# Optimization experiments

Measured on AMD Instinct MI355X. Metric: run time of the kernel, lower is better.

## Reference

```python
import jax, jax.numpy as jnp
import numpy as np

B, T, C = 4, 4096, 1024
NH, DH = 16, 128          # n_head, d_head = d_qkv // n_head
DQKV, DR = 2048, 256      # d_qkv, d_rank


def _uniform(key, shape, bound):
    return jax.random.uniform(key, shape, jnp.float32, -bound, bound)


def setup_inputs() -> dict:
    key = jax.random.key(0)
    k0, k1, k2, k3, k4 = jax.random.split(key, 5)
    # CastedLinear init: bound = sqrt(3) * 0.5 * in_features**-0.5 (same for w1, w2)
    b_qkv = (3 ** 0.5) * 0.5 * C ** (-0.5)
    b_proj = (3 ** 0.5) * 0.5 * DQKV ** (-0.5)
    return {
        "x": jax.random.normal(k0, (B, T, C), jnp.float32),
        "qkv_w1": _uniform(k1, (DR, C), b_qkv),
        "qkv_w2": _uniform(k2, (3 * DQKV, DR), b_qkv),
        "cproj_w1": _uniform(k3, (DR, DQKV), b_proj),
        "cproj_w2": _uniform(k4, (2 * C, DR), b_proj),
    }


def _rmsnorm(x):
    eps = jnp.finfo(x.dtype).eps  # F.rms_norm default eps
    return x * jax.lax.rsqrt(jnp.mean(x * x, axis=-1, keepdims=True) + eps)


def reference(x, qkv_w1, qkv_w2, cproj_w1, cproj_w2):
    Bx, Tx, Cx = x.shape
    # qkv projection with low-rank factorization + relu^2 activation between factors
    h = _rmsnorm(x) @ qkv_w1.T                      # [B,T,DR]
    h = jnp.square(jax.nn.relu(h))
    qkv = (h @ qkv_w2.T).reshape(Bx, Tx, 3 * NH, DH)
    q, k, v = jnp.split(qkv, 3, axis=2)             # each [B,T,NH,DH]
    q, k = _rmsnorm(q), _rmsnorm(k)

    # rotary embedding: half the head dim rotated, second quarter frequencies zero
    quarter = DH // 4
    freq = (1.0 / 1024.0) ** jnp.linspace(0.0, 1.0, quarter)
    freq = jnp.concatenate([freq, jnp.zeros(quarter, freq.dtype)])  # [DH//2]
    theta = jnp.arange(Tx, dtype=jnp.float32)[:, None] * freq[None, :]
    cos = jnp.cos(theta)[None, :, None, :]          # [1,T,1,DH//2]
    sin = jnp.sin(theta)[None, :, None, :]

    def rope(z):
        z1, z2 = jnp.split(z, 2, axis=-1)
        return jnp.concatenate([z1 * cos + z2 * sin, -z1 * sin + z2 * cos], axis=-1)

    q, k = rope(q), rope(k)

    # causal linear attention: sigmoid-gated cumulative sum over time
    y = jax.nn.relu(q) * jnp.cumsum(jax.nn.sigmoid(k) * v, axis=1)  # [B,T,NH,DH]
    y = y.reshape(Bx, Tx, NH * DH)

    # low-rank output projection (no activation), gated residual
    uv = (y @ cproj_w1.T) @ cproj_w2.T              # [B,T,2C]
    u, g = jnp.split(uv, 2, axis=-1)
    return x + u * jax.nn.silu(g)
```

## Files before the change

kernel.cpp:

```cpp
#include <hip/hip_runtime.h>
#include <hip/hip_bf16.h>

#define TB 4
#define TT 4096
#define TC 1024
#define TNH 16
#define TDH 128
#define TDQKV 2048
#define TDR 256
#define RB 4096
#define ROWS (TB*TT)
#define SLAB (RB*128)
#define NSEG 128
#define SEGT 32

typedef __attribute__((ext_vector_type(8))) short bfx8;
typedef __attribute__((ext_vector_type(4))) float fx4;
typedef __attribute__((address_space(1))) const unsigned char GAS;
typedef __attribute__((address_space(3))) unsigned char LAS;

__device__ __forceinline__ unsigned short f2b(float f) {
    unsigned int u = __float_as_uint(f);
    unsigned int r = (u + 0x7fffu + ((u >> 16) & 1u)) >> 16;
    return (unsigned short)r;
}
__device__ __forceinline__ float b2f(unsigned short h) {
    return __uint_as_float(((unsigned int)h) << 16);
}
__device__ __forceinline__ float sigm(float x) {
    return 1.0f / (1.0f + __expf(-x));
}
__device__ __forceinline__ int xcd_swz(int hw, int nwg) {
    int q = nwg >> 3;
    return (hw & 7) * q + (hw >> 3);
}

__global__ __launch_bounds__(256) void setup_all(const float* __restrict__ wq1, unsigned short* __restrict__ w1b,
                                                 const float* __restrict__ wq2, unsigned short* __restrict__ w2b,
                                                 const float* __restrict__ wc1, unsigned short* __restrict__ wp1b,
                                                 const float* __restrict__ wc2, unsigned short* __restrict__ wp2b,
                                                 float* __restrict__ ct, float* __restrict__ st) {
    int blk = blockIdx.x;
    if (blk < 2816) {
        const float* in; unsigned short* out; int base;
        if (blk < 256)       { in = wq1; out = w1b;  base = blk; }
        else if (blk < 1792) { in = wq2; out = w2b;  base = blk - 256; }
        else if (blk < 2304) { in = wc1; out = wp1b; base = blk - 1792; }
        else                 { in = wc2; out = wp2b; base = blk - 2304; }
        int i = (base * 256 + threadIdx.x) * 4;
        float4 v = *(const float4*)(in + i);
        out[i + 0] = f2b(v.x);
        out[i + 1] = f2b(v.y);
        out[i + 2] = f2b(v.z);
        out[i + 3] = f2b(v.w);
    } else {
        int i = (blk - 2816) * 256 + threadIdx.x;
        int t = i >> 5, j = i & 31;
        float fr = exp2f(-10.0f * (float)j / 31.0f);
        float th = (float)t * fr;
        ct[i] = cosf(th);
        st[i] = sinf(th);
    }
}

__global__ __launch_bounds__(256) void rmsnorm_x(const float* __restrict__ x,
                                                 unsigned short* __restrict__ xn) {
    int row = blockIdx.x;
    int tid = threadIdx.x;
    float4 v = *(const float4*)(x + (size_t)row * TC + tid * 4);
    float ss = v.x * v.x + v.y * v.y + v.z * v.z + v.w * v.w;
    #pragma unroll
    for (int o = 32; o > 0; o >>= 1) ss += __shfl_xor(ss, o);
    __shared__ float red[4];
    if ((tid & 63) == 0) red[tid >> 6] = ss;
    __syncthreads();
    float tot = red[0] + red[1] + red[2] + red[3];
    float sc = rsqrtf(tot * (1.0f / TC) + 1.1920929e-7f);
    unsigned short* o = xn + (size_t)row * TC + tid * 4;
    o[0] = f2b(v.x * sc); o[1] = f2b(v.y * sc); o[2] = f2b(v.z * sc); o[3] = f2b(v.w * sc);
}

template <int EPI>
__global__ __launch_bounds__(256) void gemm_bt(const unsigned short* __restrict__ A, int lda,
                                               const unsigned short* __restrict__ Bm,
                                               unsigned short* __restrict__ C, int ldc,
                                               int N, int K) {
    __shared__ unsigned short As[2][128 * 32];
    __shared__ unsigned short Bs[2][128 * 32];
    const int m0 = blockIdx.y * 128;
    const int n0 = blockIdx.x * 128;
    const int tid = threadIdx.x;
    const int lane = tid & 63;
    const int w = tid >> 6;
    const int wr = w >> 1, wc = w & 1;
    const int r16 = lane & 15;
    const int kk = (lane >> 4) * 8;
    const int l4 = lane >> 2;
    const int c8 = (lane & 3) * 8;
    const int nk = K >> 5;
    fx4 acc[4][4] = {};

    auto stage = [&](int buf, int k0) {
        #pragma unroll
        for (int i = 0; i < 2; ++i) {
            int rr = (w + 4 * i) * 16 + l4;
            const unsigned short* ga = A + (size_t)(m0 + rr) * lda + k0 + c8;
            const unsigned short* gb = Bm + (size_t)(n0 + rr) * K + k0 + c8;
            __builtin_amdgcn_global_load_lds((GAS*)ga, (LAS*)&As[buf][(w + 4 * i) * 512], 16, 0, 0);
            __builtin_amdgcn_global_load_lds((GAS*)gb, (LAS*)&Bs[buf][(w + 4 * i) * 512], 16, 0, 0);
        }
    };

    stage(0, 0);
    __syncthreads();
    int buf = 0;
    for (int ks = 0; ks < nk; ++ks) {
        if (ks + 1 < nk) stage(buf ^ 1, (ks + 1) * 32);
        bfx8 af[4], bfr[4];
        #pragma unroll
        for (int mi = 0; mi < 4; mi++) af[mi] = *(const bfx8*)&As[buf][(wr * 64 + mi * 16 + r16) * 32 + kk];
        #pragma unroll
        for (int ni = 0; ni < 4; ni++) bfr[ni] = *(const bfx8*)&Bs[buf][(wc * 64 + ni * 16 + r16) * 32 + kk];
        #pragma unroll
        for (int mi = 0; mi < 4; mi++)
            #pragma unroll
            for (int ni = 0; ni < 4; ni++)
                acc[mi][ni] = __builtin_amdgcn_mfma_f32_16x16x32_bf16(af[mi], bfr[ni], acc[mi][ni], 0, 0, 0);
        __syncthreads();
        buf ^= 1;
    }

    const int rg = lane >> 4;
    #pragma unroll
    for (int mi = 0; mi < 4; mi++)
        #pragma unroll
        for (int ni = 0; ni < 4; ni++) {
            int col = n0 + wc * 64 + ni * 16 + r16;
            #pragma unroll
            for (int r = 0; r < 4; r++) {
                int row = m0 + wr * 64 + mi * 16 + rg * 4 + r;
                float v = acc[mi][ni][r];
                if (EPI == 1) { v = fmaxf(v, 0.0f); v *= v; }
                if (EPI == 2) {
                    int head = col >> 7;
                    C[(size_t)head * SLAB + (size_t)row * 128 + (col & 127)] = f2b(v);
                } else {
                    C[(size_t)row * ldc + col] = f2b(v);
                }
            }
        }
}

template <int EPI, int NX>
__global__ __launch_bounds__(256) void gemm_sk(const unsigned short* __restrict__ A, int lda,
                                               const unsigned short* __restrict__ Bm,
                                               unsigned short* __restrict__ C, int ldc,
                                               int K) {
    __shared__ unsigned short As[2][128 * 32];
    __shared__ unsigned short Bs[2][64 * 32];
    const int lg = xcd_swz(blockIdx.x, gridDim.x);
    const int n0 = (lg % NX) * 64;
    const int m0 = (lg / NX) * 128;
    const int tid = threadIdx.x;
    const int lane = tid & 63;
    const int w = tid >> 6;
    const int wr = w >> 1, wc = w & 1;
    const int r16 = lane & 15;
    const int kk = (lane >> 4) * 8;
    const int l4 = lane >> 2;
    const int c8 = (lane & 3) * 8;
    const int nk = K >> 5;
    fx4 acc[4][2] = {};

    auto stage = [&](int buf, int k0) {
        #pragma unroll
        for (int i = 0; i < 2; ++i) {
            int rr = (w + 4 * i) * 16 + l4;
            const unsigned short* ga = A + (size_t)(m0 + rr) * lda + k0 + c8;
            __builtin_amdgcn_global_load_lds((GAS*)ga, (LAS*)&As[buf][(w + 4 * i) * 512], 16, 0, 0);
        }
        const unsigned short* gb = Bm + (size_t)(n0 + w * 16 + l4) * K + k0 + c8;
        __builtin_amdgcn_global_load_lds((GAS*)gb, (LAS*)&Bs[buf][w * 512], 16, 0, 0);
    };

    stage(0, 0);
    __syncthreads();
    int buf = 0;
    for (int ks = 0; ks < nk; ++ks) {
        if (ks + 1 < nk) stage(buf ^ 1, (ks + 1) * 32);
        bfx8 af[4], bfr[2];
        #pragma unroll
        for (int mi = 0; mi < 4; mi++) af[mi] = *(const bfx8*)&As[buf][(wr * 64 + mi * 16 + r16) * 32 + kk];
        #pragma unroll
        for (int ni = 0; ni < 2; ni++) bfr[ni] = *(const bfx8*)&Bs[buf][(wc * 32 + ni * 16 + r16) * 32 + kk];
        #pragma unroll
        for (int mi = 0; mi < 4; mi++)
            #pragma unroll
            for (int ni = 0; ni < 2; ni++)
                acc[mi][ni] = __builtin_amdgcn_mfma_f32_16x16x32_bf16(af[mi], bfr[ni], acc[mi][ni], 0, 0, 0);
        __syncthreads();
        buf ^= 1;
    }

    const int rg = lane >> 4;
    #pragma unroll
    for (int mi = 0; mi < 4; mi++)
        #pragma unroll
        for (int ni = 0; ni < 2; ni++) {
            int col = n0 + wc * 32 + ni * 16 + r16;
            #pragma unroll
            for (int r = 0; r < 4; r++) {
                int row = m0 + wr * 64 + mi * 16 + rg * 4 + r;
                float v = acc[mi][ni][r];
                if (EPI == 1) { v = fmaxf(v, 0.0f); v *= v; }
                C[(size_t)row * ldc + col] = f2b(v);
            }
        }
}

__global__ __launch_bounds__(256) void gemm4f64(const unsigned short* __restrict__ A,
                                                const unsigned short* __restrict__ Wm,
                                                const float* __restrict__ x,
                                                float* __restrict__ out) {
    __shared__ unsigned short As[2][64 * 32];
    __shared__ unsigned short Bu[2][64 * 32];
    __shared__ unsigned short Bg[2][64 * 32];
    const int hw = blockIdx.y * gridDim.x + blockIdx.x;
    const int lg = xcd_swz(hw, gridDim.x * gridDim.y);
    const int n0 = (lg & 15) * 64;
    const int m0 = (lg >> 4) * 64;
    const int tid = threadIdx.x;
    const int lane = tid & 63;
    const int w = tid >> 6;
    const int wr = w >> 1, wc = w & 1;
    const int r16 = lane & 15;
    const int rg = lane >> 4;
    const int kk = rg * 8;
    const int l4 = lane >> 2;
    const int c8 = (lane & 3) * 8;
    fx4 accu[2][2] = {};
    fx4 accg[2][2] = {};

    auto stage = [&](int buf, int k0) {
        int rr = w * 16 + l4;
        const unsigned short* ga = A + (size_t)(m0 + rr) * TDR + k0 + c8;
        const unsigned short* gu = Wm + (size_t)(n0 + rr) * TDR + k0 + c8;
        const unsigned short* gg = Wm + (size_t)(1024 + n0 + rr) * TDR + k0 + c8;
        __builtin_amdgcn_global_load_lds((GAS*)ga, (LAS*)&As[buf][w * 512], 16, 0, 0);
        __builtin_amdgcn_global_load_lds((GAS*)gu, (LAS*)&Bu[buf][w * 512], 16, 0, 0);
        __builtin_amdgcn_global_load_lds((GAS*)gg, (LAS*)&Bg[buf][w * 512], 16, 0, 0);
    };

    stage(0, 0);
    float xr[2][2][4];
    #pragma unroll
    for (int mi = 0; mi < 2; mi++)
        #pragma unroll
        for (int ni = 0; ni < 2; ni++)
            #pragma unroll
            for (int r = 0; r < 4; r++)
                xr[mi][ni][r] = x[(size_t)(m0 + wr * 32 + mi * 16 + rg * 4 + r) * TC
                                  + n0 + wc * 32 + ni * 16 + r16];
    __syncthreads();
    int buf = 0;
    for (int ks = 0; ks < 8; ++ks) {
        if (ks + 1 < 8) stage(buf ^ 1, (ks + 1) * 32);
        bfx8 af[2], bu[2], bg[2];
        #pragma unroll
        for (int mi = 0; mi < 2; mi++) af[mi] = *(const bfx8*)&As[buf][(wr * 32 + mi * 16 + r16) * 32 + kk];
        #pragma unroll
        for (int ni = 0; ni < 2; ni++) {
            bu[ni] = *(const bfx8*)&Bu[buf][(wc * 32 + ni * 16 + r16) * 32 + kk];
            bg[ni] = *(const bfx8*)&Bg[buf][(wc * 32 + ni * 16 + r16) * 32 + kk];
        }
        #pragma unroll
        for (int mi = 0; mi < 2; mi++)
            #pragma unroll
            for (int ni = 0; ni < 2; ni++) {
                accu[mi][ni] = __builtin_amdgcn_mfma_f32_16x16x32_bf16(af[mi], bu[ni], accu[mi][ni], 0, 0, 0);
                accg[mi][ni] = __builtin_amdgcn_mfma_f32_16x16x32_bf16(af[mi], bg[ni], accg[mi][ni], 0, 0, 0);
            }
        __syncthreads();
        buf ^= 1;
    }

    #pragma unroll
    for (int mi = 0; mi < 2; mi++)
        #pragma unroll
        for (int ni = 0; ni < 2; ni++) {
            int col = n0 + wc * 32 + ni * 16 + r16;
            #pragma unroll
            for (int r = 0; r < 4; r++) {
                int row = m0 + wr * 32 + mi * 16 + rg * 4 + r;
                float u = accu[mi][ni][r];
                float g = accg[mi][ni][r];
                out[(size_t)row * TC + col] = xr[mi][ni][r] + u * (g * sigm(g));
            }
        }
}

__global__ __launch_bounds__(256) void post64(unsigned short* __restrict__ qkv,
                                              const float* __restrict__ ct,
                                              const float* __restrict__ st,
                                              float* __restrict__ part) {
    const int blk = blockIdx.x;
    const int tile = blk & 63, h = blk >> 6;
    const int g = threadIdx.x >> 4, l16 = threadIdx.x & 15;
    const int d0 = l16 * 4;
    unsigned short* qs = qkv + (size_t)h * SLAB;
    unsigned short* ks = qkv + (size_t)(16 + h) * SLAB;
    unsigned short* vs = qkv + (size_t)(32 + h) * SLAB;
    __shared__ float psum[2][16][128];
    float acc0[2][4] = {};
    float acc1[2][4] = {};

    #pragma unroll
    for (int p = 0; p < 4; ++p) {
        const int t = tile * 64 + p * 16 + g;
        const size_t lo = (size_t)t * 128 + d0, hi = lo + 64;
        ushort4 q1 = *(const ushort4*)(qs + lo);
        ushort4 q2 = *(const ushort4*)(qs + hi);
        ushort4 k1 = *(const ushort4*)(ks + lo);
        ushort4 k2 = *(const ushort4*)(ks + hi);
        float qa[8] = {b2f(q1.x), b2f(q1.y), b2f(q1.z), b2f(q1.w),
                       b2f(q2.x), b2f(q2.y), b2f(q2.z), b2f(q2.w)};
        float ka[8] = {b2f(k1.x), b2f(k1.y), b2f(k1.z), b2f(k1.w),
                       b2f(k2.x), b2f(k2.y), b2f(k2.z), b2f(k2.w)};
        float ssq = 0.0f, ssk = 0.0f;
        #pragma unroll
        for (int j = 0; j < 8; ++j) { ssq += qa[j] * qa[j]; ssk += ka[j] * ka[j]; }
        #pragma unroll
        for (int o = 8; o > 0; o >>= 1) {
            ssq += __shfl_xor(ssq, o);
            ssk += __shfl_xor(ssk, o);
        }
        float qsc = rsqrtf(ssq * (1.0f / TDH) + 1.1920929e-7f);
        float ksc = rsqrtf(ssk * (1.0f / TDH) + 1.1920929e-7f);
        float c[4], s[4];
        if (l16 < 8) {
            float4 cv = *(const float4*)(ct + t * 32 + d0);
            float4 sv = *(const float4*)(st + t * 32 + d0);
            c[0] = cv.x; c[1] = cv.y; c[2] = cv.z; c[3] = cv.w;
            s[0] = sv.x; s[1] = sv.y; s[2] = sv.z; s[3] = sv.w;
        } else {
            c[0] = c[1] = c[2] = c[3] = 1.0f;
            s[0] = s[1] = s[2] = s[3] = 0.0f;
        }
        ushort4 v1 = *(const ushort4*)(vs + lo);
        ushort4 v2 = *(const ushort4*)(vs + hi);
        float va[8] = {b2f(v1.x), b2f(v1.y), b2f(v1.z), b2f(v1.w),
                       b2f(v2.x), b2f(v2.y), b2f(v2.z), b2f(v2.w)};
        ushort4 qo1, qo2, po1, po2;
        unsigned short* qo1p = (unsigned short*)&qo1;
        unsigned short* qo2p = (unsigned short*)&qo2;
        unsigned short* po1p = (unsigned short*)&po1;
        unsigned short* po2p = (unsigned short*)&po2;
        const int h2 = p >> 1;
        #pragma unroll
        for (int j = 0; j < 4; ++j) {
            float z1q = qa[j] * qsc, z2q = qa[4 + j] * qsc;
            float z1k = ka[j] * ksc, z2k = ka[4 + j] * ksc;
            float qlo = z1q * c[j] + z2q * s[j];
            float qhi = z2q * c[j] - z1q * s[j];
            float klo = z1k * c[j] + z2k * s[j];
            float khi = z2k * c[j] - z1k * s[j];
            float plo = sigm(klo) * va[j];
            float phi = sigm(khi) * va[4 + j];
            qo1p[j] = f2b(qlo); qo2p[j] = f2b(qhi);
            po1p[j] = f2b(plo); po2p[j] = f2b(phi);
            acc0[h2][j] += plo;
            acc1[h2][j] += phi;
        }
        *(ushort4*)(qs + lo) = qo1;
        *(ushort4*)(qs + hi) = qo2;
        *(ushort4*)(ks + lo) = po1;
        *(ushort4*)(ks + hi) = po2;
    }
    #pragma unroll
    for (int h2 = 0; h2 < 2; ++h2) {
        *(float4*)&psum[h2][g][d0]      = *(float4*)acc0[h2];
        *(float4*)&psum[h2][g][64 + d0] = *(float4*)acc1[h2];
    }
    __syncthreads();
    const int h2 = threadIdx.x >> 7, d = threadIdx.x & 127;
    float tot = 0.0f;
    #pragma unroll
    for (int gg = 0; gg < 16; ++gg) tot += psum[h2][gg][d];
    part[((size_t)h * NSEG + tile * 2 + h2) * 128 + d] = tot;
}

__global__ __launch_bounds__(256) void scanB128(float* __restrict__ part) {
    int idx = blockIdx.x * 256 + threadIdx.x;
    int h = idx >> 7, d = idx & 127;
    float run = 0.0f;
    #pragma unroll 8
    for (int s = 0; s < NSEG; ++s) {
        float* p = part + ((size_t)(h * NSEG + s)) * 128 + d;
        float tv = *p;
        *p = run;
        run += tv;
    }
}

__global__ __launch_bounds__(256) void scanC3(const unsigned short* __restrict__ qkv,
                                              const float* __restrict__ part,
                                              unsigned short* __restrict__ y) {
    const int bseg = blockIdx.x & 7, h = blockIdx.x >> 3;
    const int g = threadIdx.x >> 4, l16 = threadIdx.x & 15;
    const int seg = bseg * 16 + g;
    const int d0 = l16 * 8;
    const unsigned short* qp = qkv + (size_t)h * SLAB;
    const unsigned short* pp = qkv + (size_t)(16 + h) * SLAB;
    float sum[8];
    const float* pb = part + ((size_t)(h * NSEG + seg)) * 128 + d0;
    *(float4*)&sum[0] = *(const float4*)pb;
    *(float4*)&sum[4] = *(const float4*)(pb + 4);
    #pragma unroll 4
    for (int i = 0; i < SEGT; ++i) {
        int t = seg * SEGT + i;
        size_t off = (size_t)t * 128 + d0;
        bfx8 pv = *(const bfx8*)(pp + off);
        bfx8 qv = *(const bfx8*)(qp + off);
        bfx8 ov;
        #pragma unroll
        for (int j = 0; j < 8; ++j) {
            sum[j] += b2f((unsigned short)pv[j]);
            float q = b2f((unsigned short)qv[j]);
            ov[j] = (short)f2b(fmaxf(q, 0.0f) * sum[j]);
        }
        *(bfx8*)(y + (size_t)t * 2048 + h * 128 + d0) = ov;
    }
}

extern "C" void kernel_launch(void* const* d_in, const int* in_sizes, int n_in,
                              void* d_out, int out_size, void* d_ws, size_t ws_size,
                              hipStream_t stream) {
    (void)in_sizes; (void)n_in; (void)out_size; (void)ws_size;
    const float* x    = (const float*)d_in[0];
    const float* wq1  = (const float*)d_in[1];
    const float* wq2  = (const float*)d_in[2];
    const float* wc1  = (const float*)d_in[3];
    const float* wc2  = (const float*)d_in[4];
    float* out = (float*)d_out;

    char* ws = (char*)d_ws;
    size_t off = 0;
    auto alloc = [&](size_t bytes) -> void* {
        off = (off + 255) & ~(size_t)255;
        void* p = ws + off;
        off += bytes;
        return p;
    };
    char* pool = (char*)alloc((size_t)RB * 6144 * 2);
    unsigned short* qkvb = (unsigned short*)pool;
    unsigned short* xn   = (unsigned short*)pool;
    unsigned short* t1   = (unsigned short*)pool;
    unsigned short* hbuf = (unsigned short*)alloc((size_t)ROWS * TDR * 2);
    unsigned short* w1b  = (unsigned short*)alloc((size_t)TDR * TC * 2);
    unsigned short* w2b  = (unsigned short*)alloc((size_t)3 * TDQKV * TDR * 2);
    unsigned short* wp1b = (unsigned short*)alloc((size_t)TDR * TDQKV * 2);
    unsigned short* wp2b = (unsigned short*)alloc((size_t)2 * TC * TDR * 2);
    float* ct   = (float*)alloc((size_t)TT * 32 * 4);
    float* st   = (float*)alloc((size_t)TT * 32 * 4);
    float* part = (float*)alloc((size_t)TNH * NSEG * 128 * 4);
    unsigned short* ybuf = (unsigned short*)d_out;

    setup_all<<<3328, 256, 0, stream>>>(wq1, w1b, wq2, w2b, wc1, wp1b, wc2, wp2b, ct, st);

    rmsnorm_x<<<ROWS, 256, 0, stream>>>(x, xn);
    gemm_sk<1, 4><<<(ROWS / 128) * (TDR / 64), 256, 0, stream>>>(
        xn, TC, w1b, hbuf, TDR, TC);

    for (int b = 0; b < TB; ++b) {
        gemm_bt<2><<<dim3(6144 / 128, RB / 128), 256, 0, stream>>>(
            hbuf + (size_t)b * RB * TDR, TDR, w2b, qkvb, 0, 6144, TDR);
        post64<<<TNH * 64, 256, 0, stream>>>(qkvb, ct, st, part);
        scanB128<<<(TNH * 128) / 256, 256, 0, stream>>>(part);
        scanC3<<<TNH * 8, 256, 0, stream>>>(qkvb, part, ybuf + (size_t)b * RB * 2048);
    }

    gemm_sk<0, 4><<<(ROWS / 128) * (TDR / 64), 256, 0, stream>>>(
        ybuf, 2048, wp1b, t1, TDR, TDQKV);
    gemm4f64<<<dim3(TC / 64, ROWS / 64), 256, 0, stream>>>(t1, wp2b, x, out);
}
```

Measured before the change: 376.9 us.

## Process multiple batches per chunk in qkv/scan pipeline based on workspace size

Parameterizes the per-batch qkv GEMM, post, and scan kernels by a chunk size, so up to four batches are processed per launch when the workspace allows. This cuts the number of launches and gives larger grids, aiming to fill the GPU better and reduce tail effects. The scan resets its running sum every 128 segments to keep batches independent. The final gated-output GEMM now loads the residual x in the epilogue instead of prefetching it before the K loop, which lowers register pressure but exposes that load latency. The larger qkv buffer also raises workspace use and memory footprint.

```diff
diff --git a/kernel.cpp b/kernel.cpp
--- a/kernel.cpp
+++ b/kernel.cpp
@@ -10,9 +10,6 @@
 #define TDR 256
 #define RB 4096
 #define ROWS (TB*TT)
-#define SLAB (RB*128)
-#define NSEG 128
-#define SEGT 32
 
 typedef __attribute__((ext_vector_type(8))) short bfx8;
 typedef __attribute__((ext_vector_type(4))) float fx4;
@@ -84,7 +81,7 @@
 __global__ __launch_bounds__(256) void gemm_bt(const unsigned short* __restrict__ A, int lda,
                                                const unsigned short* __restrict__ Bm,
                                                unsigned short* __restrict__ C, int ldc,
-                                               int N, int K) {
+                                               int N, int K, size_t slab) {
     __shared__ unsigned short As[2][128 * 32];
     __shared__ unsigned short Bs[2][128 * 32];
     const int m0 = blockIdx.y * 128;
@@ -143,7 +140,7 @@
                 if (EPI == 1) { v = fmaxf(v, 0.0f); v *= v; }
                 if (EPI == 2) {
                     int head = col >> 7;
-                    C[(size_t)head * SLAB + (size_t)row * 128 + (col & 127)] = f2b(v);
+                    C[(size_t)head * slab + (size_t)row * 128 + (col & 127)] = f2b(v);
                 } else {
                     C[(size_t)row * ldc + col] = f2b(v);
                 }
@@ -234,8 +231,7 @@
     const int w = tid >> 6;
     const int wr = w >> 1, wc = w & 1;
     const int r16 = lane & 15;
-    const int rg = lane >> 4;
-    const int kk = rg * 8;
+    const int kk = (lane >> 4) * 8;
     const int l4 = lane >> 2;
     const int c8 = (lane & 3) * 8;
     fx4 accu[2][2] = {};
@@ -252,15 +248,6 @@
     };
 
     stage(0, 0);
-    float xr[2][2][4];
-    #pragma unroll
-    for (int mi = 0; mi < 2; mi++)
-        #pragma unroll
-        for (int ni = 0; ni < 2; ni++)
-            #pragma unroll
-            for (int r = 0; r < 4; r++)
-                xr[mi][ni][r] = x[(size_t)(m0 + wr * 32 + mi * 16 + rg * 4 + r) * TC
-                                  + n0 + wc * 32 + ni * 16 + r16];
     __syncthreads();
     int buf = 0;
     for (int ks = 0; ks < 8; ++ks) {
@@ -284,6 +271,7 @@
         buf ^= 1;
     }
 
+    const int rg = lane >> 4;
     #pragma unroll
     for (int mi = 0; mi < 2; mi++)
         #pragma unroll
@@ -294,7 +282,8 @@
                 int row = m0 + wr * 32 + mi * 16 + rg * 4 + r;
                 float u = accu[mi][ni][r];
                 float g = accg[mi][ni][r];
-                out[(size_t)row * TC + col] = xr[mi][ni][r] + u * (g * sigm(g));
+                size_t idx = (size_t)row * TC + col;
+                out[idx] = x[idx] + u * (g * sigm(g));
             }
         }
 }
@@ -302,22 +291,25 @@
 __global__ __launch_bounds__(256) void post64(unsigned short* __restrict__ qkv,
                                               const float* __restrict__ ct,
                                               const float* __restrict__ st,
-                                              float* __restrict__ part) {
+                                              float* __restrict__ part,
+                                              int ntiles, int nseg) {
     const int blk = blockIdx.x;
-    const int tile = blk & 63, h = blk >> 6;
+    const int tile = blk % ntiles, h = blk / ntiles;
+    const size_t slab = (size_t)ntiles * 64 * 128;
     const int g = threadIdx.x >> 4, l16 = threadIdx.x & 15;
     const int d0 = l16 * 4;
-    unsigned short* qs = qkv + (size_t)h * SLAB;
-    unsigned short* ks = qkv + (size_t)(16 + h) * SLAB;
-    unsigned short* vs = qkv + (size_t)(32 + h) * SLAB;
+    unsigned short* qs = qkv + (size_t)h * slab;
+    unsigned short* ks = qkv + (size_t)(16 + h) * slab;
+    unsigned short* vs = qkv + (size_t)(32 + h) * slab;
     __shared__ float psum[2][16][128];
     float acc0[2][4] = {};
     float acc1[2][4] = {};
 
     #pragma unroll
     for (int p = 0; p < 4; ++p) {
-        const int t = tile * 64 + p * 16 + g;
-        const size_t lo = (size_t)t * 128 + d0, hi = lo + 64;
+        const int r = tile * 64 + p * 16 + g;
+        const int t = r & (TT - 1);
+        const size_t lo = (size_t)r * 128 + d0, hi = lo + 64;
         ushort4 q1 = *(const ushort4*)(qs + lo);
         ushort4 q2 = *(const ushort4*)(qs + hi);
         ushort4 k1 = *(const ushort4*)(ks + lo);
@@ -386,16 +378,16 @@
     float tot = 0.0f;
     #pragma unroll
     for (int gg = 0; gg < 16; ++gg) tot += psum[h2][gg][d];
-    part[((size_t)h * NSEG + tile * 2 + h2) * 128 + d] = tot;
-}
-
-__global__ __launch_bounds__(256) void scanB128(float* __restrict__ part) {
+    part[((size_t)h * nseg + tile * 2 + h2) * 128 + d] = tot;
+}
+
+__global__ __launch_bounds__(256) void scanB128(float* __restrict__ part, int nseg) {
     int idx = blockIdx.x * 256 + threadIdx.x;
     int h = idx >> 7, d = idx & 127;
     float run = 0.0f;
-    #pragma unroll 8
-    for (int s = 0; s < NSEG; ++s) {
-        float* p = part + ((size_t)(h * NSEG + s)) * 128 + d;
+    for (int s = 0; s < nseg; ++s) {
+        if ((s & 127) == 0) run = 0.0f;
+        float* p = part + ((size_t)h * nseg + s) * 128 + d;
         float tv = *p;
         *p = run;
         run += tv;
@@ -404,20 +396,22 @@
 
 __global__ __launch_bounds__(256) void scanC3(const unsigned short* __restrict__ qkv,
                                               const float* __restrict__ part,
-                                              unsigned short* __restrict__ y) {
-    const int bseg = blockIdx.x & 7, h = blockIdx.x >> 3;
+                                              unsigned short* __restrict__ y,
+                                              int nsegblk, int nseg) {
+    const int bseg = blockIdx.x % nsegblk, h = blockIdx.x / nsegblk;
+    const size_t slab = (size_t)nseg * 32 * 128;
     const int g = threadIdx.x >> 4, l16 = threadIdx.x & 15;
     const int seg = bseg * 16 + g;
     const int d0 = l16 * 8;
-    const unsigned short* qp = qkv + (size_t)h * SLAB;
-    const unsigned short* pp = qkv + (size_t)(16 + h) * SLAB;
+    const unsigned short* qp = qkv + (size_t)h * slab;
+    const unsigned short* pp = qkv + (size_t)(16 + h) * slab;
     float sum[8];
-    const float* pb = part + ((size_t)(h * NSEG + seg)) * 128 + d0;
+    const float* pb = part + ((size_t)h * nseg + seg) * 128 + d0;
     *(float4*)&sum[0] = *(const float4*)pb;
     *(float4*)&sum[4] = *(const float4*)(pb + 4);
     #pragma unroll 4
-    for (int i = 0; i < SEGT; ++i) {
-        int t = seg * SEGT + i;
+    for (int i = 0; i < 32; ++i) {
+        int t = seg * 32 + i;
         size_t off = (size_t)t * 128 + d0;
         bfx8 pv = *(const bfx8*)(pp + off);
         bfx8 qv = *(const bfx8*)(qp + off);
@@ -435,13 +429,35 @@
 extern "C" void kernel_launch(void* const* d_in, const int* in_sizes, int n_in,
                               void* d_out, int out_size, void* d_ws, size_t ws_size,
                               hipStream_t stream) {
-    (void)in_sizes; (void)n_in; (void)out_size; (void)ws_size;
+    (void)in_sizes; (void)n_in; (void)out_size;
     const float* x    = (const float*)d_in[0];
     const float* wq1  = (const float*)d_in[1];
     const float* wq2  = (const float*)d_in[2];
     const float* wc1  = (const float*)d_in[3];
     const float* wc2  = (const float*)d_in[4];
     float* out = (float*)d_out;
+
+    auto need = [](int cb) -> size_t {
+        size_t o = 0;
+        auto a = [&](size_t b) { o = (o + 255) & ~(size_t)255; o += b; };
+        size_t qkvsz = (size_t)cb * RB * 6144 * 2;
+        size_t xnsz  = (size_t)ROWS * TC * 2;
+        a(qkvsz > xnsz ? qkvsz : xnsz);
+        a((size_t)ROWS * TDR * 2);
+        a((size_t)TDR * TC * 2);
+        a((size_t)3 * TDQKV * TDR * 2);
+        a((size_t)TDR * TDQKV * 2);
+        a((size_t)2 * TC * TDR * 2);
+        a((size_t)TT * 32 * 4);
+        a((size_t)TT * 32 * 4);
+        a((size_t)TNH * (cb * RB / 32) * 128 * 4);
+        return o;
+    };
+    int CB = (ws_size >= need(4)) ? 4 : (ws_size >= need(2)) ? 2 : 1;
+    const int TR = CB * RB;
+    const int NCH = TB / CB;
+    const int nseg = TR / 32;
+    const int ntiles = TR / 64;
 
     char* ws = (char*)d_ws;
     size_t off = 0;
@@ -451,7 +467,9 @@
         off += bytes;
         return p;
     };
-    char* pool = (char*)alloc((size_t)RB * 6144 * 2);
+    size_t qkvsz = (size_t)TR * 6144 * 2;
+    size_t xnsz  = (size_t)ROWS * TC * 2;
+    char* pool = (char*)alloc(qkvsz > xnsz ? qkvsz : xnsz);
     unsigned short* qkvb = (unsigned short*)pool;
     unsigned short* xn   = (unsigned short*)pool;
     unsigned short* t1   = (unsigned short*)pool;
@@ -462,7 +480,7 @@
     unsigned short* wp2b = (unsigned short*)alloc((size_t)2 * TC * TDR * 2);
     float* ct   = (float*)alloc((size_t)TT * 32 * 4);
     float* st   = (float*)alloc((size_t)TT * 32 * 4);
-    float* part = (float*)alloc((size_t)TNH * NSEG * 128 * 4);
+    float* part = (float*)alloc((size_t)TNH * nseg * 128 * 4);
     unsigned short* ybuf = (unsigned short*)d_out;
 
     setup_all<<<3328, 256, 0, stream>>>(wq1, w1b, wq2, w2b, wc1, wp1b, wc2, wp2b, ct, st);
@@ -471,12 +489,13 @@
     gemm_sk<1, 4><<<(ROWS / 128) * (TDR / 64), 256, 0, stream>>>(
         xn, TC, w1b, hbuf, TDR, TC);
 
-    for (int b = 0; b < TB; ++b) {
-        gemm_bt<2><<<dim3(6144 / 128, RB / 128), 256, 0, stream>>>(
-            hbuf + (size_t)b * RB * TDR, TDR, w2b, qkvb, 0, 6144, TDR);
-        post64<<<TNH * 64, 256, 0, stream>>>(qkvb, ct, st, part);
-        scanB128<<<(TNH * 128) / 256, 256, 0, stream>>>(part);
-        scanC3<<<TNH * 8, 256, 0, stream>>>(qkvb, part, ybuf + (size_t)b * RB * 2048);
+    for (int c = 0; c < NCH; ++c) {
+        gemm_bt<2><<<dim3(6144 / 128, TR / 128), 256, 0, stream>>>(
+            hbuf + (size_t)c * TR * TDR, TDR, w2b, qkvb, 0, 6144, TDR, (size_t)TR * 128);
+        post64<<<TNH * ntiles, 256, 0, stream>>>(qkvb, ct, st, part, ntiles, nseg);
+        scanB128<<<(TNH * 128) / 256, 256, 0, stream>>>(part, nseg);
+        scanC3<<<TNH * (nseg / 16), 256, 0, stream>>>(
+            qkvb, part, ybuf + (size_t)c * TR * 2048, nseg / 16, nseg);
     }
 
     gemm_sk<0, 4><<<(ROWS / 128) * (TDR / 64), 256, 0, stream>>>(
```

Measured after the change: 465.5 us. +23.5%, slower.
